# Optimization experiments

Hardware: AMD Instinct MI355X
Metric: run time of the kernel (lower is better)

## Reference

```python
import jax, jax.numpy as jnp
import numpy as np

N_HEAD = 4
N_FEAT = 256
D_K = N_FEAT // N_HEAD
SCALE = 1.0  # self.scale (non-trainable, scale>0 and tr_scale=None)
INV_SQRT_DK = 1.0 / (D_K ** 0.5)


def sparsemax(z, scale=1.0):
    """Closed-form equivalent of the module's sort-based sparsemax loop.
    Projects onto the simplex of radius `scale`, then divides by scale.
    Matches the strict `>` support condition of the while-loop."""
    n = z.shape[-1]
    z_sorted = jnp.flip(jnp.sort(z, axis=-1), axis=-1)          # descending
    csum = jnp.cumsum(z_sorted, axis=-1)
    k = jnp.arange(1, n + 1, dtype=z.dtype)
    support = k * z_sorted > (csum - scale)                      # strict, as in torch loop
    k_max = jnp.sum(support, axis=-1, keepdims=True)             # int, >=1 in practice
    csum_k = jnp.take_along_axis(csum, k_max - 1, axis=-1)
    tau = (csum_k - scale) / k_max.astype(z.dtype)               # tau_z
    return jax.nn.relu(z - tau) / scale


def setup_inputs() -> dict:
    key = jax.random.key(0)
    ks = jax.random.split(key, 9)
    B, T1, T2 = 4, 2048, 2048
    query = jax.random.normal(ks[0], (B, T1, N_FEAT), jnp.float32)
    key_t = jax.random.normal(ks[1], (B, T2, N_FEAT), jnp.float32)
    value = jax.random.normal(ks[2], (B, T2, N_FEAT), jnp.float32)
    mask = jnp.ones((B, 1, T2), jnp.int32)
    s = 0.02
    Wq = jax.random.normal(ks[3], (N_FEAT, N_FEAT), jnp.float32) * s
    bq = jax.random.normal(ks[4], (N_FEAT,), jnp.float32) * s
    Wk = jax.random.normal(ks[5], (N_FEAT, N_FEAT), jnp.float32) * s
    bk = jax.random.normal(ks[6], (N_FEAT,), jnp.float32) * s
    Wv = jax.random.normal(ks[7], (N_FEAT, N_FEAT), jnp.float32) * s
    bv = jax.random.normal(ks[8], (N_FEAT,), jnp.float32) * s
    return {"query": query, "key": key_t, "value": value, "mask": mask,
            "Wq": Wq, "bq": bq, "Wk": Wk, "bk": bk, "Wv": Wv, "bv": bv}


def reference(query, key, value, mask, Wq, bq, Wk, bk, Wv, bv):
    B, T1, _ = query.shape
    # forward_qkv: project, split heads, L2-normalize q/k (cosine attention) * scale
    q = (query @ Wq.T + bq).reshape(B, T1, N_HEAD, D_K).transpose(0, 2, 1, 3)  # (B,H,T1,dk)
    k = (key @ Wk.T + bk).reshape(B, -1, N_HEAD, D_K).transpose(0, 2, 1, 3)    # (B,H,T2,dk)
    v = (value @ Wv.T + bv).reshape(B, -1, N_HEAD, D_K).transpose(0, 2, 1, 3)  # (B,H,T2,dk)
    q = q / jnp.linalg.norm(q, axis=-1, keepdims=True) * SCALE
    k = k / jnp.linalg.norm(k, axis=-1, keepdims=True) * SCALE
    scores = jnp.einsum('bhqd,bhkd->bhqk', q, k) * INV_SQRT_DK  # (B,H,T1,T2)
    # forward_attention with mask: fill masked with float min, sparsemax, zero masked
    m = (mask[:, None, :, :] == 0)                               # (B,1,1|T1,T2)
    min_val = jnp.finfo(scores.dtype).min
    scores = jnp.where(m, min_val, scores)
    attn = jnp.where(m, 0.0, sparsemax(scores, 1.0))
    x = jnp.einsum('bhqk,bhkd->bhqd', attn, v)
    x = x.transpose(0, 2, 1, 3).reshape(B, T1, N_HEAD * D_K)     # NOTE: linear_out is never applied in the original forward
    return attn, x
```

## Files before the change

### kernel.cpp

```cpp
#include <hip/hip_runtime.h>
#include <hip/hip_bf16.h>

#define NB 4
#define NH 4
#define TT 2048
#define DKK 64
#define NF 256
#define QT 16

typedef __attribute__((ext_vector_type(8))) short bf16x8;
typedef __attribute__((ext_vector_type(4))) short s16x4;
typedef __attribute__((ext_vector_type(4))) float f32x4;
typedef __hip_bfloat16 bf16;

__device__ __forceinline__ short f2bs(float f) {
    bf16 h = __float2bfloat16(f);
    return *reinterpret_cast<short*>(&h);
}
__device__ __forceinline__ float b2f(short s) {
    return __uint_as_float(((unsigned)(unsigned short)s) << 16);
}
__device__ __forceinline__ float wave_sum(float v) {
    #pragma unroll
    for (int off = 1; off < 64; off <<= 1) v += __shfl_xor(v, off);
    return v;
}
__device__ __forceinline__ void lds_barrier() {
    asm volatile("s_waitcnt lgkmcnt(0)" ::: "memory");
    __builtin_amdgcn_s_barrier();
    __builtin_amdgcn_sched_barrier(0);
}

__global__ __launch_bounds__(256)
void wcvt_kernel(const float* __restrict__ Wq, const float* __restrict__ Wk,
                 const float* __restrict__ Wv, const int* __restrict__ mask,
                 bf16* __restrict__ Wb, unsigned* __restrict__ mbits)
{
    if (blockIdx.x == 192) {
        int t = threadIdx.x;
        const int* mp = mask + t * 32;
        unsigned m = 0;
        #pragma unroll
        for (int j = 0; j < 32; ++j) m |= (mp[j] != 0 ? 1u : 0u) << j;
        mbits[t] = m;
        return;
    }
    int gid = (blockIdx.x * 256 + threadIdx.x) * 4;
    const float* src;
    int m = gid >> 16, off = gid & 65535;
    src = (m == 0) ? Wq : (m == 1) ? Wk : Wv;
    float4 v = *(const float4*)(src + off);
    s16x4 o = { f2bs(v.x), f2bs(v.y), f2bs(v.z), f2bs(v.w) };
    *(s16x4*)((short*)Wb + gid) = o;
}

__global__ __launch_bounds__(256, 4)
void qkv_kernel(const float* __restrict__ query, const float* __restrict__ key,
                const float* __restrict__ value, const bf16* __restrict__ Wb,
                const float* __restrict__ bq, const float* __restrict__ bk,
                const float* __restrict__ bv,
                bf16* __restrict__ qB, bf16* __restrict__ kA, bf16* __restrict__ vB)
{
    __shared__ char Xq[8192], Xk[8192], Xv[8192];
    __shared__ char bounce[24576];
    const int tid = threadIdx.x;
    const int bt0 = blockIdx.x * 16;
    const int b0 = bt0 >> 11, t0 = bt0 & (TT - 1);

    {
        int row = tid >> 4, c0 = (tid & 15) * 16;
        int swr = (row & 7) << 4;
        const float* qs = query + (size_t)(bt0 + row) * NF + c0;
        const float* ks = key   + (size_t)(bt0 + row) * NF + c0;
        const float* vs = value + (size_t)(bt0 + row) * NF + c0;
        #pragma unroll
        for (int j = 0; j < 4; ++j) {
            float4 a = *(const float4*)(qs + j * 4);
            float4 b = *(const float4*)(ks + j * 4);
            float4 c = *(const float4*)(vs + j * 4);
            int byt = (row * 512 + c0 * 2 + j * 8) ^ swr;
            *(s16x4*)(Xq + byt) = (s16x4){ f2bs(a.x), f2bs(a.y), f2bs(a.z), f2bs(a.w) };
            *(s16x4*)(Xk + byt) = (s16x4){ f2bs(b.x), f2bs(b.y), f2bs(b.z), f2bs(b.w) };
            *(s16x4*)(Xv + byt) = (s16x4){ f2bs(c.x), f2bs(c.y), f2bs(c.z), f2bs(c.w) };
        }
    }
    __syncthreads();

    const int lane = tid & 63;
    const int w = tid >> 6;
    const int l15 = lane & 15;
    const int g = lane >> 4;
    const int swl = (l15 & 7) << 4;

    f32x4 qa[4], ka[4], va[4];
    #pragma unroll
    for (int ct = 0; ct < 4; ++ct) {
        qa[ct] = (f32x4){0.f,0.f,0.f,0.f};
        ka[ct] = (f32x4){0.f,0.f,0.f,0.f};
        va[ct] = (f32x4){0.f,0.f,0.f,0.f};
    }
    const bf16* Wqb = Wb;
    const bf16* Wkb = Wb + 65536;
    const bf16* Wvb = Wb + 131072;

    #pragma unroll
    for (int kt = 0; kt < 8; ++kt) {
        int byt = (l15 * 512 + kt * 64 + g * 16) ^ swl;
        bf16x8 xq = *(const bf16x8*)(Xq + byt);
        bf16x8 xk = *(const bf16x8*)(Xk + byt);
        bf16x8 xv = *(const bf16x8*)(Xv + byt);
        #pragma unroll
        for (int ct = 0; ct < 4; ++ct) {
            size_t wo = (size_t)(w * 64 + ct * 16 + l15) * NF + kt * 32 + g * 8;
            bf16x8 aq = *(const bf16x8*)(Wqb + wo);
            bf16x8 ak = *(const bf16x8*)(Wkb + wo);
            bf16x8 av = *(const bf16x8*)(Wvb + wo);
            qa[ct] = __builtin_amdgcn_mfma_f32_16x16x32_bf16(aq, xq, qa[ct], 0, 0, 0);
            ka[ct] = __builtin_amdgcn_mfma_f32_16x16x32_bf16(ak, xk, ka[ct], 0, 0, 0);
            va[ct] = __builtin_amdgcn_mfma_f32_16x16x32_bf16(av, xv, va[ct], 0, 0, 0);
        }
    }

    float qv[4][4], kv[4][4], vv[4][4];
    float sq = 0.f, sk = 0.f;
    #pragma unroll
    for (int ct = 0; ct < 4; ++ct) {
        float4 b4q = *(const float4*)(bq + w * 64 + ct * 16 + g * 4);
        float4 b4k = *(const float4*)(bk + w * 64 + ct * 16 + g * 4);
        float4 b4v = *(const float4*)(bv + w * 64 + ct * 16 + g * 4);
        #pragma unroll
        for (int p = 0; p < 4; ++p) {
            float bqp = (p == 0) ? b4q.x : (p == 1) ? b4q.y : (p == 2) ? b4q.z : b4q.w;
            float bkp = (p == 0) ? b4k.x : (p == 1) ? b4k.y : (p == 2) ? b4k.z : b4k.w;
            float bvp = (p == 0) ? b4v.x : (p == 1) ? b4v.y : (p == 2) ? b4v.z : b4v.w;
            qv[ct][p] = qa[ct][p] + bqp;
            kv[ct][p] = ka[ct][p] + bkp;
            vv[ct][p] = va[ct][p] + bvp;
            sq = __builtin_fmaf(qv[ct][p], qv[ct][p], sq);
            sk = __builtin_fmaf(kv[ct][p], kv[ct][p], sk);
        }
    }
    sq += __shfl_xor(sq, 16); sq += __shfl_xor(sq, 32);
    sk += __shfl_xor(sk, 16); sk += __shfl_xor(sk, 32);
    float nq = rsqrtf(sq) * 0.125f;
    float nk = rsqrtf(sk);

    __syncthreads();
    #pragma unroll
    for (int ct = 0; ct < 4; ++ct) {
        #pragma unroll
        for (int p = 0; p < 4; ++p) {
            int d5 = (ct & 1) * 16 + g * 4 + p;
            int qb = w * 2048 + (ct >> 1) * 1024 + (d5 >> 3) * 256 + l15 * 16 + (d5 & 7) * 2;
            *(short*)(bounce + qb)        = f2bs(qv[ct][p] * nq);
            *(short*)(bounce + qb + 8192) = f2bs(kv[ct][p] * nk);
            int vb = 16384 + w * 2048 + ct * 512 + (l15 >> 3) * 256 + (g * 4 + p) * 16 + (l15 & 7) * 2;
            *(short*)(bounce + vb)        = f2bs(vv[ct][p]);
        }
    }
    __syncthreads();

    const int qt = t0 >> 4;
    const int kc = t0 >> 5, h16 = (t0 >> 4) & 1;
    for (int seg = tid; seg < 1536; seg += 256) {
        int byt = seg * 16;
        const char* src = bounce + byt;
        bf16* dst;
        if (byt < 8192) {
            int wh = byt >> 11, off = byt & 2047;
            dst = qB + (((size_t)(b0 * NH + wh)) * 128 + qt) * 1024 + off / 2;
        } else if (byt < 16384) {
            int r = byt - 8192;
            int wh = r >> 11, off = r & 2047;
            dst = kA + (((size_t)(b0 * NH + wh)) * 128 + qt) * 1024 + off / 2;
        } else {
            int r = byt - 16384;
            int wh = r >> 11, ct = (r >> 9) & 3, off = r & 511;
            dst = vB + ((((size_t)(b0 * NH + wh)) * 64 + kc) * 4 + ct) * 512 + h16 * 256 + off / 2;
        }
        *(bf16x8*)dst = *(const bf16x8*)src;
    }
}

__global__ __launch_bounds__(512, 4)
void attn_kernel(const bf16* __restrict__ qB, const bf16* __restrict__ kA,
                 const bf16* __restrict__ vB, const unsigned* __restrict__ mbits,
                 float* __restrict__ attn, float* __restrict__ xout)
{
    __shared__ short S_s[16 * 2048];
    __shared__ float4 xpart[4][64];
    const int tid = threadIdx.x;
    const int lane = tid & 63;
    const int w = tid >> 6;
    const int l15 = lane & 15;
    const int g = lane >> 4;
    const int swz = (blockIdx.x & 7) * 256 + (blockIdx.x >> 3);
    const int bh = swz >> 7;
    const int qt = swz & 127;
    const int q0 = qt * QT;
    const int b_ = bh >> 2, h_ = bh & 3;

    const size_t fb = (size_t)bh * 16384;
    const bf16x8* qBv = (const bf16x8*)qB + fb + (size_t)qt * 128;
    const bf16x8* kAv = (const bf16x8*)kA + fb;
    const bf16x8* vBv = (const bf16x8*)vB + fb;

    unsigned mreg[8];
    {
        const unsigned* mwp = mbits + b_ * 64 + w * 8;
        #pragma unroll
        for (int i = 0; i < 8; ++i) mreg[i] = mwp[i];
    }

    bf16x8 qf0 = qBv[lane];
    bf16x8 qf1 = qBv[64 + lane];

    f32x4 acc[16];
    #pragma unroll
    for (int t = 0; t < 16; ++t) acc[t] = (f32x4){0.f, 0.f, 0.f, 0.f};

    #pragma unroll
    for (int t = 0; t < 16; ++t) {
        int kt = w * 16 + t;
        bf16x8 kf0 = kAv[(kt * 2 + 0) * 64 + lane];
        bf16x8 kf1 = kAv[(kt * 2 + 1) * 64 + lane];
        acc[t] = __builtin_amdgcn_mfma_f32_16x16x32_bf16(kf0, qf0, acc[t], 0, 0, 0);
        acc[t] = __builtin_amdgcn_mfma_f32_16x16x32_bf16(kf1, qf1, acc[t], 0, 0, 0);
    }

    const short NEGB = (short)0xFF7F;
    char* prow = (char*)S_s + l15 * 4096;
    const int sw = (l15 & 7) << 4;
    #pragma unroll
    for (int t = 0; t < 16; ++t) {
        unsigned bits = mreg[t >> 1] >> (((t & 1) << 4) + (g << 2));
        s16x4 sb;
        sb[0] = (bits & 1) ? f2bs(acc[t][0]) : NEGB;
        sb[1] = (bits & 2) ? f2bs(acc[t][1]) : NEGB;
        sb[2] = (bits & 4) ? f2bs(acc[t][2]) : NEGB;
        sb[3] = (bits & 8) ? f2bs(acc[t][3]) : NEGB;
        *(s16x4*)(prow + ((w * 512 + t * 32 + g * 8) ^ sw)) = sb;
    }
    __syncthreads();

    const int r0 = 2 * w;
    float va[2][32];
    #pragma unroll
    for (int h = 0; h < 2; ++h) {
        const char* sr = (const char*)S_s + (r0 + h) * 4096;
        int swr = ((r0 + h) & 7) << 4;
        #pragma unroll
        for (int jj = 0; jj < 8; ++jj) {
            s16x4 p4 = *(const s16x4*)(sr + ((jj * 512 + lane * 8) ^ swr));
            va[h][jj * 4 + 0] = b2f(p4[0]);
            va[h][jj * 4 + 1] = b2f(p4[1]);
            va[h][jj * 4 + 2] = b2f(p4[2]);
            va[h][jj * 4 + 3] = b2f(p4[3]);
        }
    }

    float tau[2];
    #pragma unroll
    for (int h = 0; h < 2; ++h) {
        float S = 0.f, C = 0.f, Qs = 0.f;
        #pragma unroll
        for (int i = 0; i < 32; ++i) {
            float v = va[h][i];
            bool un = v > -1.0e30f;
            float sv = un ? v : 0.f;
            S += sv;
            C += un ? 1.f : 0.f;
            Qs = __builtin_fmaf(sv, sv, Qs);
        }
        S = wave_sum(S); C = wave_sum(C); Qs = wave_sum(Qs);
        float tu, prevC;
        bool done;
        if (C < 0.5f) { tu = 3.0e38f; done = true; prevC = 0.f; }
        else {
            float mu = S / C;
            float var = Qs / C - mu * mu;
            var = var > 0.f ? var : 0.f;
            tu = mu + 1.7f * __builtin_sqrtf(var);
            prevC = -1.f;
            done = false;
        }
        for (int it = 0; it < 64 && !done; ++it) {
            float S2 = 0.f, C2 = 0.f;
            #pragma unroll
            for (int i = 0; i < 32; ++i) {
                float v = va[h][i];
                bool in = v > tu;
                S2 += in ? v : 0.f;
                C2 += in ? 1.f : 0.f;
            }
            S2 = wave_sum(S2); C2 = wave_sum(C2);
            if (C2 == prevC) done = true;
            else if (C2 < 0.5f) { tu = (S - 1.f) / C; prevC = -1.f; }
            else { tu = (S2 - 1.f) / C2; prevC = C2; }
        }
        tau[h] = tu;
    }

    #pragma unroll
    for (int h = 0; h < 2; ++h) {
        char* sr = (char*)S_s + (r0 + h) * 4096;
        int swr = ((r0 + h) & 7) << 4;
        float* ar = attn + ((size_t)bh * TT + q0 + r0 + h) * TT;
        float tu = tau[h];
        #pragma unroll
        for (int jj = 0; jj < 8; ++jj) {
            f32x4 o;
            s16x4 pb4;
            #pragma unroll
            for (int e = 0; e < 4; ++e) {
                float a = va[h][jj * 4 + e] - tu;
                a = a > 0.f ? a : 0.f;
                o[e] = a;
                pb4[e] = f2bs(a);
            }
            __builtin_nontemporal_store(o, (f32x4*)(ar + jj * 256 + lane * 4));
            *(s16x4*)(sr + ((jj * 512 + lane * 8) ^ swr)) = pb4;
        }
    }
    lds_barrier();

    const int ds = w & 3;
    const int kh = w >> 2;
    f32x4 xacc = (f32x4){0.f, 0.f, 0.f, 0.f};
    __builtin_amdgcn_s_setprio(1);
    #pragma unroll 8
    for (int kcl = 0; kcl < 32; ++kcl) {
        int kc = kh * 32 + kcl;
        bf16x8 af = *(const bf16x8*)(prow + ((kh * 2048 + kcl * 64 + g * 16) ^ sw));
        bf16x8 bfr = vBv[(kc * 4 + ds) * 64 + lane];
        xacc = __builtin_amdgcn_mfma_f32_16x16x32_bf16(af, bfr, xacc, 0, 0, 0);
    }
    __builtin_amdgcn_s_setprio(0);
    if (w >= 4) xpart[w - 4][lane] = make_float4(xacc[0], xacc[1], xacc[2], xacc[3]);
    lds_barrier();
    if (w < 4) {
        float4 xp4 = xpart[w][lane];
        xacc[0] += xp4.x; xacc[1] += xp4.y; xacc[2] += xp4.z; xacc[3] += xp4.w;
        float* xp = xout + ((size_t)b_ * TT + q0 + g * 4) * NF + h_ * DKK + ds * 16 + l15;
        #pragma unroll
        for (int p = 0; p < 4; ++p)
            __builtin_nontemporal_store(xacc[p], xp + p * NF);
    }
}

extern "C" void kernel_launch(void* const* d_in, const int* in_sizes, int n_in,
                              void* d_out, int out_size, void* d_ws, size_t ws_size,
                              hipStream_t stream) {
    const float* query = (const float*)d_in[0];
    const float* key   = (const float*)d_in[1];
    const float* value = (const float*)d_in[2];
    const int*   mask  = (const int*)d_in[3];
    const float* Wq = (const float*)d_in[4];
    const float* bq = (const float*)d_in[5];
    const float* Wk = (const float*)d_in[6];
    const float* bk = (const float*)d_in[7];
    const float* Wv = (const float*)d_in[8];
    const float* bv = (const float*)d_in[9];

    float* attn = (float*)d_out;
    float* x    = (float*)d_out + (size_t)NB * NH * TT * TT;

    const size_t FRAG = (size_t)NB * NH * 16384 * 8;
    bf16* Wb = (bf16*)d_ws;
    bf16* qB = Wb + 3 * 65536;
    bf16* kA = qB + FRAG;
    bf16* vB = kA + FRAG;
    unsigned* mbits = (unsigned*)(vB + FRAG);

    wcvt_kernel<<<dim3(193), dim3(256), 0, stream>>>(Wq, Wk, Wv, mask, Wb, mbits);
    qkv_kernel<<<dim3(NB * TT / 16), dim3(256), 0, stream>>>(
        query, key, value, Wb, bq, bk, bv, qB, kA, vB);
    attn_kernel<<<dim3(NB * NH * (TT / QT)), dim3(512), 0, stream>>>(
        qB, kA, vB, mbits, attn, x);
}
```

Measured before the change: 135.0 us.

## Defer fp32 attn stores until after the PV matmul, reading them back from LDS

The fp32 attention rows are no longer stored right after the sparsemax threshold. They are written at the end of the kernel by reading the bf16 probabilities back from the LDS score buffer, so the PV MFMA loop is not queued behind heavy global stores. The per-element q/k bounce-buffer writes become 4-wide vector stores, and one __syncthreads is replaced by an LDS-only barrier. In exchange, the attn output now holds bf16-rounded probabilities instead of exact fp32 values, and the extra LDS reads could stretch the kernel tail.

```diff
diff --git a/kernel.cpp b/kernel.cpp
--- a/kernel.cpp
+++ b/kernel.cpp
@@ -148,14 +148,16 @@
     __syncthreads();
     #pragma unroll
     for (int ct = 0; ct < 4; ++ct) {
+        int d5 = (ct & 1) * 16 + g * 4;
+        int qb = w * 2048 + (ct >> 1) * 1024 + (d5 >> 3) * 256 + l15 * 16 + (d5 & 7) * 2;
+        s16x4 oq = { f2bs(qv[ct][0]*nq), f2bs(qv[ct][1]*nq), f2bs(qv[ct][2]*nq), f2bs(qv[ct][3]*nq) };
+        s16x4 ok = { f2bs(kv[ct][0]*nk), f2bs(kv[ct][1]*nk), f2bs(kv[ct][2]*nk), f2bs(kv[ct][3]*nk) };
+        *(s16x4*)(bounce + qb)        = oq;
+        *(s16x4*)(bounce + qb + 8192) = ok;
         #pragma unroll
         for (int p = 0; p < 4; ++p) {
-            int d5 = (ct & 1) * 16 + g * 4 + p;
-            int qb = w * 2048 + (ct >> 1) * 1024 + (d5 >> 3) * 256 + l15 * 16 + (d5 & 7) * 2;
-            *(short*)(bounce + qb)        = f2bs(qv[ct][p] * nq);
-            *(short*)(bounce + qb + 8192) = f2bs(kv[ct][p] * nk);
             int vb = 16384 + w * 2048 + ct * 512 + (l15 >> 3) * 256 + (g * 4 + p) * 16 + (l15 & 7) * 2;
-            *(short*)(bounce + vb)        = f2bs(vv[ct][p]);
+            *(short*)(bounce + vb) = f2bs(vv[ct][p]);
         }
     }
     __syncthreads();
@@ -241,7 +243,7 @@
         sb[3] = (bits & 8) ? f2bs(acc[t][3]) : NEGB;
         *(s16x4*)(prow + ((w * 512 + t * 32 + g * 8) ^ sw)) = sb;
     }
-    __syncthreads();
+    lds_barrier();
 
     const int r0 = 2 * w;
     float va[2][32];
@@ -305,20 +307,16 @@
     for (int h = 0; h < 2; ++h) {
         char* sr = (char*)S_s + (r0 + h) * 4096;
         int swr = ((r0 + h) & 7) << 4;
-        float* ar = attn + ((size_t)bh * TT + q0 + r0 + h) * TT;
         float tu = tau[h];
         #pragma unroll
         for (int jj = 0; jj < 8; ++jj) {
-            f32x4 o;
             s16x4 pb4;
             #pragma unroll
             for (int e = 0; e < 4; ++e) {
                 float a = va[h][jj * 4 + e] - tu;
                 a = a > 0.f ? a : 0.f;
-                o[e] = a;
                 pb4[e] = f2bs(a);
             }
-            __builtin_nontemporal_store(o, (f32x4*)(ar + jj * 256 + lane * 4));
             *(s16x4*)(sr + ((jj * 512 + lane * 8) ^ swr)) = pb4;
         }
     }
@@ -345,6 +343,25 @@
         #pragma unroll
         for (int p = 0; p < 4; ++p)
             __builtin_nontemporal_store(xacc[p], xp + p * NF);
+    }
+
+    {
+        int row = 2 * w + (lane >> 5);
+        int c0 = (lane & 31) * 4;
+        const char* pr = (const char*)S_s + row * 4096;
+        int swr = (row & 7) << 4;
+        float* ar = attn + ((size_t)bh * TT + q0 + row) * TT;
+        #pragma unroll
+        for (int i = 0; i < 16; ++i) {
+            int c = c0 + i * 128;
+            uint2 pk = *(const uint2*)(pr + ((c * 2) ^ swr));
+            f32x4 o;
+            o[0] = __uint_as_float(pk.x << 16);
+            o[1] = __uint_as_float(pk.x & 0xffff0000u);
+            o[2] = __uint_as_float(pk.y << 16);
+            o[3] = __uint_as_float(pk.y & 0xffff0000u);
+            __builtin_nontemporal_store(o, (f32x4*)(ar + c));
+        }
     }
 }
 
```

Measured after the change: 142.2 us. 1.05x slower.
